# Performance work log

Hardware: AMD Instinct MI355X
Metric: run time of the kernel (lower is better)

The kernel has to match this reference:

```python
import jax, jax.numpy as jnp
import numpy as np
from jax import lax

SR = 16000
N_FFT = 400
HOP = 200
N_MELS = 128
HID = 128


def _mel_fb():
    # torchaudio melscale_fbanks defaults: htk scale, norm=None, f_min=0, f_max=sr/2
    all_freqs = np.linspace(0.0, SR / 2, N_FFT // 2 + 1)  # (201,)
    hz2mel = lambda f: 2595.0 * np.log10(1.0 + f / 700.0)
    mel2hz = lambda m: 700.0 * (10.0 ** (m / 2595.0) - 1.0)
    m_pts = np.linspace(hz2mel(0.0), hz2mel(SR / 2), N_MELS + 2)
    f_pts = mel2hz(m_pts)  # (130,)
    f_diff = np.diff(f_pts)  # (129,)
    slopes = f_pts[None, :] - all_freqs[:, None]  # (201,130)
    down = -slopes[:, :-2] / f_diff[:-1]
    up = slopes[:, 2:] / f_diff[1:]
    fb = np.maximum(0.0, np.minimum(down, up))  # (201,128)
    return jnp.asarray(fb, dtype=jnp.float32)

MEL_FB = _mel_fb()
HANN = jnp.asarray(np.hanning(N_FFT + 1)[:-1], dtype=jnp.float32)  # periodic hann(400)


def mel_spectrogram(x):
    # x: (B, T) waveform -> (B, n_mels, frames), power=2 mel spectrogram
    pad = N_FFT // 2
    xp = jnp.pad(x, ((0, 0), (pad, pad)), mode='reflect')
    n_frames = 1 + (xp.shape[1] - N_FFT) // HOP  # 81 for T=16000
    idx = jnp.arange(n_frames)[:, None] * HOP + jnp.arange(N_FFT)[None, :]
    frames = xp[:, idx] * HANN  # (B, frames, 400)
    spec = jnp.fft.rfft(frames, axis=-1)  # (B, frames, 201)
    power = jnp.abs(spec) ** 2
    mel = power @ MEL_FB  # (B, frames, 128)
    return jnp.transpose(mel, (0, 2, 1))  # (B, 128, frames)


def lstm_layer(x, W, U, b):
    # x: (B, T, F); gate order i, f, g, o (matches torch slicing)
    B = x.shape[0]
    h0 = jnp.zeros((B, HID), x.dtype)
    c0 = jnp.zeros((B, HID), x.dtype)

    def step(carry, x_t):
        h, c = carry
        gates = x_t @ W + h @ U + b  # (B, 4H)
        i = jax.nn.sigmoid(gates[:, :HID])
        f = jax.nn.sigmoid(gates[:, HID:2 * HID])
        g = jnp.tanh(gates[:, 2 * HID:3 * HID])
        o = jax.nn.sigmoid(gates[:, 3 * HID:])
        c = f * c + i * g
        h = o * jnp.tanh(c)
        return (h, c), h

    _, hs = lax.scan(step, (h0, c0), jnp.transpose(x, (1, 0, 2)))  # (T, B, H)
    return jnp.transpose(hs, (1, 0, 2))  # (B, T, H)


def setup_inputs() -> dict:
    key = jax.random.key(0)
    ks = jax.random.split(key, 16)
    s = 0.05
    return {
        'x': jax.random.normal(ks[0], (1024, 16000), dtype=jnp.float32),
        'conv_w': jax.random.normal(ks[1], (128, 128, 3), dtype=jnp.float32) * s,  # (out,in,k)
        'conv_b': jax.random.normal(ks[2], (128,), dtype=jnp.float32) * s,
        'W1': jax.random.normal(ks[3], (128, 4 * HID), dtype=jnp.float32) * s,
        'U1': jax.random.normal(ks[4], (HID, 4 * HID), dtype=jnp.float32) * s,
        'b1': jax.random.normal(ks[5], (4 * HID,), dtype=jnp.float32) * s,
        'W2': jax.random.normal(ks[6], (HID, 4 * HID), dtype=jnp.float32) * s,
        'U2': jax.random.normal(ks[7], (HID, 4 * HID), dtype=jnp.float32) * s,
        'b2': jax.random.normal(ks[8], (4 * HID,), dtype=jnp.float32) * s,
        'fc1_w': jax.random.normal(ks[9], (128, 128), dtype=jnp.float32) * s,  # (in,out)
        'fc1_b': jax.random.normal(ks[10], (128,), dtype=jnp.float32) * s,
        'proj_w': jax.random.normal(ks[11], (128, 35), dtype=jnp.float32) * s,  # (in,out)
        'proj_b': jax.random.normal(ks[12], (35,), dtype=jnp.float32) * s,
    }


def reference(x, conv_w, conv_b, W1, U1, b1, W2, U2, b2, fc1_w, fc1_b, proj_w, proj_b):
    # MelSpectrogram -> Conv1d(128,128,3) -> permute -> LSTM x2 -> fc1 -> mean(time) -> proj
    spec = mel_spectrogram(x)  # (B, 128, 81)
    conv = lax.conv_general_dilated(
        spec, conv_w, window_strides=(1,), padding='VALID',
        dimension_numbers=('NCH', 'OIH', 'NCH')) + conv_b[None, :, None]  # (B,128,79)
    h = jnp.transpose(conv, (0, 2, 1))  # (B, 79, 128)
    h = lstm_layer(h, W1, U1, b1)
    h = lstm_layer(h, W2, U2, b2)
    h = h @ fc1_w + fc1_b  # (B, 79, 128)
    h = jnp.mean(h, axis=1)  # (B, 128)
    return h @ proj_w + proj_b  # (B, 35)
```

## Files before the change

### kernel.cpp

```cpp
#include <hip/hip_runtime.h>
#include <math.h>

#define PI_D 3.14159265358979323846

#define BATCH   1024
#define TLEN    16000
#define NFFT    400
#define HOP     200
#define NFRAME  81
#define NBIN    201
#define NMEL    128
#define HID     128
#define TSTEPS  79
#define GATES   512

#define KDFT    416
#define NDFT    512
#define SINOFF  256
#define KPOW    224
#define KCONV   384
#define NCHUNK  2
#define CHROWS  (BATCH*NFRAME/NCHUNK)

static inline size_t al512(size_t v){ return (v + 511) & ~((size_t)511); }

__device__ __forceinline__ unsigned short bf_rne(float f){
    unsigned u = __float_as_uint(f);
    u += 0x7FFF + ((u >> 16) & 1);
    return (unsigned short)(u >> 16);
}
__device__ __forceinline__ void bf_split(float f, unsigned short& h, unsigned short& l){
    h = bf_rne(f);
    float hf = __uint_as_float(((unsigned)h) << 16);
    l = bf_rne(f - hf);
}
__device__ __forceinline__ void bf_split_fast(float f, unsigned short& h, unsigned short& l){
    unsigned u = __float_as_uint(f);
    h = (unsigned short)(u >> 16);
    float hf = __uint_as_float(u & 0xFFFF0000u);
    l = (unsigned short)(__float_as_uint(f - hf) >> 16);
}

__device__ __forceinline__ int kswz(int n, int k){
    return (k & ~31) | (((((k >> 3) & 3) ^ ((n >> 1) & 3))) << 3) | (k & 7);
}

typedef short bf16x8 __attribute__((ext_vector_type(8)));
typedef float f32x4  __attribute__((ext_vector_type(4)));
typedef unsigned short us8 __attribute__((ext_vector_type(8)));
typedef unsigned short us4 __attribute__((ext_vector_type(4)));
typedef _Float16 f16x8 __attribute__((ext_vector_type(8)));

__device__ __forceinline__ void gld16(const unsigned short* g, unsigned short* l){
    __builtin_amdgcn_global_load_lds(
        (const __attribute__((address_space(1))) unsigned int*)g,
        (__attribute__((address_space(3))) unsigned int*)l, 16, 0, 0);
}

__device__ __forceinline__ void barrier_lds(){
    __builtin_amdgcn_sched_barrier(0);
    asm volatile("s_waitcnt lgkmcnt(0)" ::: "memory");
    __builtin_amdgcn_s_barrier();
    __builtin_amdgcn_sched_barrier(0);
}

__global__ void setup_dft_t(unsigned short* __restrict__ th, unsigned short* __restrict__ tl){
    int idx = blockIdx.x*256 + threadIdx.x;
    if (idx >= NDFT*KDFT) return;
    int n = idx / KDFT, k = idx % KDFT;
    double v = 0.0;
    if (k < 400) {
        double w = 0.5 - 0.5*cos(2.0*PI_D*(double)k/400.0);
        if (n < NBIN)                              v = w * cos(2.0*PI_D*(double)((k*n)%400)/400.0);
        else if (n >= SINOFF && n < SINOFF + NBIN) v = w * sin(2.0*PI_D*(double)((k*(n-SINOFF))%400)/400.0);
    }
    unsigned short h, l; bf_split((float)v, h, l);
    int o = n*KDFT + kswz(n, k);
    th[o] = h; tl[o] = l;
}

__global__ void setup_fb_t(unsigned short* __restrict__ fh, unsigned short* __restrict__ fl){
    int idx = blockIdx.x*256 + threadIdx.x;
    if (idx >= NMEL*KPOW) return;
    int m = idx / KPOW, f = idx % KPOW;
    float v = 0.f;
    if (f < NBIN) {
        double melmax = 2595.0 * log10(1.0 + 8000.0/700.0);
        double p0 = 700.0*(pow(10.0, melmax*(double)(m  )/129.0/2595.0) - 1.0);
        double p1 = 700.0*(pow(10.0, melmax*(double)(m+1)/129.0/2595.0) - 1.0);
        double p2 = 700.0*(pow(10.0, melmax*(double)(m+2)/129.0/2595.0) - 1.0);
        double freq = 40.0 * (double)f;
        double dn = (freq - p0)/(p1 - p0);
        double up = (p2 - freq)/(p2 - p1);
        double t  = dn < up ? dn : up;
        if (t < 0.0) t = 0.0;
        v = (float)t;
    }
    unsigned short h, l; bf_split(v, h, l);
    int o = m*KPOW + kswz(m, f);
    fh[o] = h; fl[o] = l;
}

__global__ void setup_wc_t(unsigned short* __restrict__ wh, unsigned short* __restrict__ wl,
                           const float* __restrict__ cw){
    int idx = blockIdx.x*256 + threadIdx.x;
    if (idx >= NMEL*KCONV) return;
    int o = idx / KCONV, kk = idx % KCONV;
    int ksh = kk >> 7, i = kk & 127;
    unsigned short h, l; bf_split(cw[o*384 + i*3 + ksh], h, l);
    int p = o*KCONV + kswz(o, kk);
    wh[p] = h; wl[p] = l;
}

__global__ void setup_w_t(unsigned short* __restrict__ wh, unsigned short* __restrict__ wl,
                          const float* __restrict__ w){
    int idx = blockIdx.x*256 + threadIdx.x;
    if (idx >= GATES*HID) return;
    int c = idx / HID, i = idx % HID;
    unsigned short h, l; bf_split(w[(size_t)i*GATES + c], h, l);
    int p = c*HID + kswz(c, i);
    wh[p] = h; wl[p] = l;
}

__global__ void setup_comb(float* __restrict__ cwm, float* __restrict__ cb,
                           const float* __restrict__ fc1w, const float* __restrict__ fc1b,
                           const float* __restrict__ projw, const float* __restrict__ projb){
    int idx = blockIdx.x*256 + threadIdx.x;
    if (idx < 128*64) {
        int i = idx / 64, o = idx % 64;
        float v = 0.f;
        if (o < 35) {
            double s = 0.0;
            for (int m = 0; m < 128; m++) s += (double)fc1w[i*128+m] * (double)projw[m*35+o];
            v = (float)s;
        }
        cwm[idx] = v;
    } else if (idx < 128*64 + 64) {
        int o = idx - 128*64;
        float v = 0.f;
        if (o < 35) {
            double s = (double)projb[o];
            for (int m = 0; m < 128; m++) s += (double)fc1b[m] * (double)projw[m*35+o];
            v = (float)s;
        }
        cb[o] = v;
    }
}

__global__ void setup_uf(_Float16* __restrict__ uf, const float* __restrict__ u){
    int idx = blockIdx.x*256 + threadIdx.x;
    if (idx >= 65536) return;
    int j    = idx & 7;
    int lane = (idx >> 3) & 63;
    int nt   = (idx >> 9) & 7;
    int ks   = (idx >> 12) & 3;
    int w    = (idx >> 14) & 3;
    int k = ks*32 + (lane >> 4)*8 + j;
    int c = w*128 + nt*16 + (lane & 15);
    uf[idx] = (_Float16)u[(size_t)k*GATES + c];
}

enum AMode { A_NORMAL=0, A_FRAMES=1, A_POWER=2, A_CONV3=3 };

template<int AMODE, bool BIAS, int NT, bool WIDE>
__global__ __launch_bounds__(256)
void mgemm_k(const float* __restrict__ A,
             const unsigned short* __restrict__ BTh, const unsigned short* __restrict__ BTl,
             const float* __restrict__ bias, float* __restrict__ C,
             int Ksteps, int lda, int kstride, int ldc,
             const float* __restrict__ aux, int rowbase)
{
    constexpr int BM = WIDE ? 64 : 128;
    constexpr int BN = WIDE ? 256 : 128;
    constexpr int AP = BM / 32;
    __shared__ unsigned short Ash[2][BM][32], Asl[2][BM][32];
    __shared__ unsigned short Bsh[2][BN][32], Bsl[2][BN][32];

    const int nwg = gridDim.x;
    const int qq = nwg >> 3, rmd = nwg & 7;
    const int xcd = blockIdx.x & 7, loc = blockIdx.x >> 3;
    const int swz = (xcd < rmd ? xcd*(qq+1) : rmd*(qq+1) + (xcd - rmd)*qq) + loc;
    constexpr int LGNT = (NT == 4) ? 2 : (NT == 2) ? 1 : 0;
    const int m0 = (swz >> LGNT) * BM;
    const int n0 = (swz & (NT-1)) * BN;

    const int tid = threadIdx.x;
    const int lane = tid & 63, w = tid >> 6;
    const int wr = WIDE ? 0 : (w >> 1) * 64;
    const int wc = WIDE ? w * 64 : (w & 1) * 64;
    const int l15 = lane & 15;
    const int swf = ((lane & 15) >> 1) & 3;
    const int pos = (((lane >> 4) ^ swf) << 3);

    const int sr  = tid >> 3;
    const int wcol = (((((tid & 7) >> 1)) ^ ((tid >> 4) & 3)) << 3) + ((tid & 1) << 2);

    float va0[AP*4], vb0[AP*4], va1[AP*4], vb1[AP*4];

    auto issue_loads = [&](float (&va)[AP*4], float (&vb)[AP*4], int ksn){
        const int k0n = ksn * 32;
        #pragma unroll
        for (int p = 0; p < AP; p++) {
            const int row = p*32 + sr;
            const int kk = k0n + (tid & 7)*4;
            if constexpr (AMODE == A_NORMAL) {
                *(float4*)&va[p*4] = *(const float4*)(A + (size_t)(m0+row)*lda + kk);
            } else if constexpr (AMODE == A_POWER) {
                const float* src = A + (size_t)(m0+row)*lda + kk;
                *(float4*)&va[p*4] = *(const float4*)(src);
                *(float4*)&vb[p*4] = *(const float4*)(src + SINOFF);
            } else if constexpr (AMODE == A_FRAMES) {
                const int rr = rowbase + m0 + row;
                const int b = rr / NFRAME, f = rr - b*NFRAME;
                const float* xb = aux + (size_t)b * TLEN;
                const int q0 = f*HOP + kk - 200;
                if (q0 >= 0 && q0 + 3 < TLEN) {
                    *(float4*)&va[p*4] = *(const float4*)(xb + q0);
                } else {
                    #pragma unroll
                    for (int j = 0; j < 4; j++) {
                        int q = q0 + j;
                        if (q < 0) q = -q;
                        else if (q >= TLEN) q = 2*TLEN - 2 - q;
                        va[p*4+j] = xb[q];
                    }
                }
            } else {
                const int rr = m0 + row;
                const int b = rr / TSTEPS, t = rr - b*TSTEPS;
                const int ksh = kk >> 7, i = kk & 127;
                *(float4*)&va[p*4] = *(const float4*)(aux + ((size_t)(b*NFRAME + t + ksh)*NMEL + i));
            }
        }
        (void)vb;
    };
    auto write_stage = [&](float (&va)[AP*4], float (&vb)[AP*4], int wb){
        #pragma unroll
        for (int p = 0; p < AP; p++) {
            const int row = p*32 + sr;
            us4 hv, lv;
            #pragma unroll
            for (int j = 0; j < 4; j++) {
                float f = va[p*4+j];
                if constexpr (AMODE == A_POWER) f = f*f + vb[p*4+j]*vb[p*4+j];
                unsigned short h, l; bf_split_fast(f, h, l);
                hv[j] = h; lv[j] = l;
            }
            *(us4*)&Ash[wb][row][wcol] = hv;
            *(us4*)&Asl[wb][row][wcol] = lv;
        }
        (void)vb;
    };
    auto dma_b = [&](int wb, int ksn){
        const int k0n = ksn * 32;
        if constexpr (WIDE) {
            #pragma unroll
            for (int p = 0; p < 4; p++) {
                const int row = w*64 + p*16;
                const size_t o = (size_t)(n0 + row + (lane >> 2))*kstride + k0n + (lane & 3)*8;
                gld16(BTh + o, &Bsh[wb][row][0]);
                gld16(BTl + o, &Bsl[wb][row][0]);
            }
        } else {
            #pragma unroll
            for (int p = 0; p < 2; p++) {
                const int row = p*64 + w*16;
                const size_t o = (size_t)(n0 + row + (lane >> 2))*kstride + k0n + (lane & 3)*8;
                gld16(BTh + o, &Bsh[wb][row][0]);
                gld16(BTl + o, &Bsl[wb][row][0]);
            }
        }
    };

    f32x4 acc[4][4] = {};

    issue_loads(va1, vb1, 0);
    dma_b(0, 0);
    write_stage(va1, vb1, 0);
    issue_loads(va0, vb0, 1);
    __syncthreads();

    auto iter = [&](int ks, float (&vac)[AP*4], float (&vbc)[AP*4],
                    float (&vao)[AP*4], float (&vbo)[AP*4], int bufc){
        const bool pf1 = (ks + 1 < Ksteps);
        const bool pf2 = (ks + 2 < Ksteps);
        if (pf2) issue_loads(vao, vbo, ks + 2);
        if (pf1) dma_b(bufc ^ 1, ks + 1);

        bf16x8 ah[4], al[4];
        #pragma unroll
        for (int mt = 0; mt < 4; mt++) {
            ah[mt] = *(const bf16x8*)&Ash[bufc][wr + mt*16 + l15][pos];
            al[mt] = *(const bf16x8*)&Asl[bufc][wr + mt*16 + l15][pos];
        }
        #pragma unroll
        for (int nt = 0; nt < 4; nt++) {
            const int nr = wc + nt*16 + l15;
            bf16x8 bh = *(const bf16x8*)&Bsh[bufc][nr][pos];
            bf16x8 bl = *(const bf16x8*)&Bsl[bufc][nr][pos];
            #pragma unroll
            for (int mt = 0; mt < 4; mt++) {
                acc[mt][nt] = __builtin_amdgcn_mfma_f32_16x16x32_bf16(ah[mt], bh, acc[mt][nt], 0, 0, 0);
                acc[mt][nt] = __builtin_amdgcn_mfma_f32_16x16x32_bf16(ah[mt], bl, acc[mt][nt], 0, 0, 0);
                acc[mt][nt] = __builtin_amdgcn_mfma_f32_16x16x32_bf16(al[mt], bh, acc[mt][nt], 0, 0, 0);
            }
        }

        if (pf1) {
            write_stage(vac, vbc, bufc ^ 1);
            __syncthreads();
        }
    };

    for (int ks = 0; ks < Ksteps; ks += 2) {
        iter(ks, va0, vb0, va1, vb1, 0);
        if (ks + 1 < Ksteps) iter(ks + 1, va1, vb1, va0, vb0, 1);
    }

    const int quad = lane >> 4;
    #pragma unroll
    for (int nt = 0; nt < 4; nt++) {
        const int col = n0 + wc + (nt << 4) + l15;
        float b = 0.f;
        if constexpr (BIAS) b = bias[col];
        #pragma unroll
        for (int mt = 0; mt < 4; mt++) {
            #pragma unroll
            for (int r = 0; r < 4; r++) {
                const int row = m0 + wr + (mt << 4) + quad*4 + r;
                C[(size_t)row*ldc + col] = acc[mt][nt][r] + b;
            }
        }
    }
}

__global__ __launch_bounds__(256)
void gemm_small(const float* __restrict__ A, const float* __restrict__ Bm,
                const float* __restrict__ bias, float* __restrict__ C,
                int M, int N, int K, int lda, int ldb, int ldc)
{
    __shared__ float As[16][64+4];
    __shared__ float Bs[16][64];
    const int tid = threadIdx.x;
    const int tx = tid & 15, ty = tid >> 4;
    const int m0 = blockIdx.x * 64;
    float acc[4][4] = {{0,0,0,0},{0,0,0,0},{0,0,0,0},{0,0,0,0}};
    const int am = tid >> 2, ak = (tid & 3) * 4;
    const int bk = tid >> 4, bn = (tid & 15) * 4;
    for (int k0 = 0; k0 < K; k0 += 16) {
        float4 av = *(const float4*)(A + (size_t)(m0+am)*lda + k0 + ak);
        As[ak+0][am]=av.x; As[ak+1][am]=av.y; As[ak+2][am]=av.z; As[ak+3][am]=av.w;
        *(float4*)&Bs[bk][bn] = *(const float4*)(Bm + (size_t)(k0+bk)*ldb + bn);
        __syncthreads();
        #pragma unroll
        for (int k = 0; k < 16; k++) {
            float4 a = *(const float4*)&As[k][ty*4];
            float4 b = *(const float4*)&Bs[k][tx*4];
            #pragma unroll
            for (int i = 0; i < 4; i++) {
                float av_ = ((const float*)&a)[i];
                acc[i][0] = fmaf(av_, b.x, acc[i][0]);
                acc[i][1] = fmaf(av_, b.y, acc[i][1]);
                acc[i][2] = fmaf(av_, b.z, acc[i][2]);
                acc[i][3] = fmaf(av_, b.w, acc[i][3]);
            }
        }
        __syncthreads();
    }
    #pragma unroll
    for (int ir = 0; ir < 4; ir++) {
        const int row = m0 + ty*4 + ir;
        #pragma unroll
        for (int jc = 0; jc < 4; jc++) {
            const int col = tx*4 + jc;
            if (col < N) C[(size_t)row*ldc + col] = acc[ir][jc] + bias[col];
        }
    }
}

__device__ __forceinline__ float sigm_f(float x){ return 1.f/(1.f + __expf(-x)); }
__device__ __forceinline__ float tanh_f(float x){ float e = __expf(2.f*x); return 1.f - 2.f/(e + 1.f); }

#define LROWS 2
#define LTHREADS 256
#define HPAD 136

__global__ __launch_bounds__(LTHREADS, 2)
void lstm_k(const float* __restrict__ X, const _Float16* __restrict__ Uf, float* __restrict__ H)
{
    __shared__ _Float16 hsA[16*HPAD];
    __shared__ float gs[GATES*5];
    const int tid = threadIdx.x;
    const int b0 = blockIdx.x * LROWS;
    const int lane = tid & 63, w = tid >> 6;
    const int m16 = lane & 15, quad = lane >> 4;
    const int r = tid >> 7;
    const int j = tid & 127;

    f32x4 bfr[4][8];
    #pragma unroll
    for (int ks = 0; ks < 4; ks++)
        #pragma unroll
        for (int nt = 0; nt < 8; nt++) {
            bfr[ks][nt] = *(const f32x4*)(Uf + ((((w*4 + ks)*8 + nt)*64 + lane) << 3));
            asm volatile("" : "+v"(bfr[ks][nt]));
        }

    for (int i = tid; i < 16*HPAD; i += LTHREADS) hsA[i] = (_Float16)0.f;
    float cst = 0.f;
    const float* xb = X + ((size_t)(b0 + r)*TSTEPS)*GATES + j;
    __syncthreads();

    float xi = xb[0], xf = xb[128], xg = xb[256], xo = xb[384];

    for (int t = 0; t < TSTEPS; t++) {
        float xi_n = 0.f, xf_n = 0.f, xg_n = 0.f, xo_n = 0.f;
        if (t + 1 < TSTEPS) {
            const float* xp = xb + (size_t)(t + 1)*GATES;
            xi_n = xp[0]; xf_n = xp[128]; xg_n = xp[256]; xo_n = xp[384];
        }

        f16x8 ah[4];
        #pragma unroll
        for (int ks = 0; ks < 4; ks++)
            ah[ks] = *(const f16x8*)&hsA[m16*HPAD + ks*32 + quad*8];

        f32x4 acc[8] = {};
        #pragma unroll
        for (int ks = 0; ks < 4; ks++)
            #pragma unroll
            for (int nt = 0; nt < 8; nt++)
                acc[nt] = __builtin_amdgcn_mfma_f32_16x16x32_f16(
                    ah[ks], __builtin_bit_cast(f16x8, bfr[ks][nt]), acc[nt], 0, 0, 0);

        if (quad == 0) {
            #pragma unroll
            for (int nt = 0; nt < 8; nt++) {
                const int c = w*128 + nt*16 + m16;
                #pragma unroll
                for (int rr = 0; rr < LROWS; rr++) gs[c*5 + rr] = acc[nt][rr];
            }
        }
        barrier_lds();

        {
            const float gi = gs[(      j)*5 + r] + xi;
            const float gf = gs[(128 + j)*5 + r] + xf;
            const float gg = gs[(256 + j)*5 + r] + xg;
            const float go = gs[(384 + j)*5 + r] + xo;
            const float cn = sigm_f(gf)*cst + sigm_f(gi)*tanh_f(gg);
            cst = cn;
            const float hn = sigm_f(go)*tanh_f(cn);
            H[((size_t)(b0 + r)*TSTEPS + t)*HID + j] = hn;
            hsA[r*HPAD + j] = (_Float16)hn;
        }
        barrier_lds();

        xi = xi_n; xf = xf_n; xg = xg_n; xo = xo_n;
    }
}

__global__ void mean_k(const float* __restrict__ H, float* __restrict__ Mh){
    const int idx = blockIdx.x*256 + threadIdx.x;
    if (idx >= BATCH*HID) return;
    const int b = idx >> 7, j = idx & 127;
    const float* p = H + (size_t)b*TSTEPS*HID + j;
    float s = 0.f;
    for (int t = 0; t < TSTEPS; t++) s += p[(size_t)t*HID];
    Mh[idx] = s * (1.0f/(float)TSTEPS);
}

extern "C" void kernel_launch(void* const* d_in, const int* in_sizes, int n_in,
                              void* d_out, int out_size, void* d_ws, size_t ws_size,
                              hipStream_t stream)
{
    const float* x      = (const float*)d_in[0];
    const float* conv_w = (const float*)d_in[1];
    const float* conv_b = (const float*)d_in[2];
    const float* W1     = (const float*)d_in[3];
    const float* U1     = (const float*)d_in[4];
    const float* b1     = (const float*)d_in[5];
    const float* W2     = (const float*)d_in[6];
    const float* U2     = (const float*)d_in[7];
    const float* b2     = (const float*)d_in[8];
    const float* fc1_w  = (const float*)d_in[9];
    const float* fc1_b  = (const float*)d_in[10];
    const float* proj_w = (const float*)d_in[11];
    const float* proj_b = (const float*)d_in[12];
    float* out = (float*)d_out;

    char* ws = (char*)d_ws;
    size_t off = 0;
    unsigned short* Tth = (unsigned short*)(ws + off); off = al512(off + (size_t)NDFT*KDFT*2);
    unsigned short* Ttl = (unsigned short*)(ws + off); off = al512(off + (size_t)NDFT*KDFT*2);
    unsigned short* fbh = (unsigned short*)(ws + off); off = al512(off + (size_t)NMEL*KPOW*2);
    unsigned short* fbl = (unsigned short*)(ws + off); off = al512(off + (size_t)NMEL*KPOW*2);
    unsigned short* wch = (unsigned short*)(ws + off); off = al512(off + (size_t)NMEL*KCONV*2);
    unsigned short* wcl = (unsigned short*)(ws + off); off = al512(off + (size_t)NMEL*KCONV*2);
    unsigned short* w1h = (unsigned short*)(ws + off); off = al512(off + (size_t)GATES*HID*2);
    unsigned short* w1l = (unsigned short*)(ws + off); off = al512(off + (size_t)GATES*HID*2);
    unsigned short* w2h = (unsigned short*)(ws + off); off = al512(off + (size_t)GATES*HID*2);
    unsigned short* w2l = (unsigned short*)(ws + off); off = al512(off + (size_t)GATES*HID*2);
    float* Cw   = (float*)(ws + off); off = al512(off + (size_t)128*64*4);
    float* Cb   = (float*)(ws + off); off = al512(off + (size_t)64*4);
    float* Mh   = (float*)(ws + off); off = al512(off + (size_t)BATCH*HID*4);
    _Float16* Uf1 = (_Float16*)(ws + off); off = al512(off + (size_t)65536*2);
    _Float16* Uf2 = (_Float16*)(ws + off); off = al512(off + (size_t)65536*2);
    float* MEL  = (float*)(ws + off); off = al512(off + (size_t)BATCH*NFRAME*NMEL*4);
    float* CONV = (float*)(ws + off); off = al512(off + (size_t)BATCH*TSTEPS*NMEL*4);
    float* X    = (float*)(ws + off); off = al512(off + (size_t)BATCH*TSTEPS*GATES*4);
    float* DFT = X;
    float* H1  = MEL;
    float* H2  = CONV;
    (void)ws_size; (void)out_size; (void)n_in; (void)in_sizes;

    setup_dft_t<<<(NDFT*KDFT + 255)/256, 256, 0, stream>>>(Tth, Ttl);
    setup_fb_t <<<(NMEL*KPOW + 255)/256, 256, 0, stream>>>(fbh, fbl);
    setup_wc_t <<<(NMEL*KCONV + 255)/256, 256, 0, stream>>>(wch, wcl, conv_w);
    setup_w_t  <<<(GATES*HID + 255)/256, 256, 0, stream>>>(w1h, w1l, W1);
    setup_w_t  <<<(GATES*HID + 255)/256, 256, 0, stream>>>(w2h, w2l, W2);
    setup_comb <<<(128*64 + 64 + 255)/256, 256, 0, stream>>>(Cw, Cb, fc1_w, fc1_b, proj_w, proj_b);
    setup_uf   <<<65536/256, 256, 0, stream>>>(Uf1, U1);
    setup_uf   <<<65536/256, 256, 0, stream>>>(Uf2, U2);

    for (int ch = 0; ch < NCHUNK; ch++) {
        const int rowbase = ch * CHROWS;
        mgemm_k<A_FRAMES,false,2,true><<<(CHROWS/64)*2, 256, 0, stream>>>(
            nullptr, Tth, Ttl, nullptr, DFT, KDFT/32, 0, KDFT, NDFT, x, rowbase);
        mgemm_k<A_POWER,false,1,false><<<CHROWS/128, 256, 0, stream>>>(
            DFT, fbh, fbl, nullptr, MEL + (size_t)rowbase*NMEL, KPOW/32, NDFT, KPOW, NMEL, nullptr, 0);
    }

    mgemm_k<A_CONV3,true,1,false><<<BATCH*TSTEPS/128, 256, 0, stream>>>(
        nullptr, wch, wcl, conv_b, CONV, KCONV/32, 0, KCONV, NMEL, MEL, 0);

    mgemm_k<A_NORMAL,true,2,true><<<(BATCH*TSTEPS/64)*2, 256, 0, stream>>>(
        CONV, w1h, w1l, b1, X, HID/32, NMEL, HID, GATES, nullptr, 0);
    lstm_k<<<BATCH/LROWS, LTHREADS, 0, stream>>>(X, Uf1, H1);

    mgemm_k<A_NORMAL,true,2,true><<<(BATCH*TSTEPS/64)*2, 256, 0, stream>>>(
        H1, w2h, w2l, b2, X, HID/32, HID, HID, GATES, nullptr, 0);
    lstm_k<<<BATCH/LROWS, LTHREADS, 0, stream>>>(X, Uf2, H2);

    mean_k<<<(BATCH*HID + 255)/256, 256, 0, stream>>>(H2, Mh);
    gemm_small<<<BATCH/64, 256, 0, stream>>>(Mh, Cw, Cb, out, BATCH, 35, HID, HID, 64, 35);
}
```

Baseline: 665.4 us.

## Interleave LSTM gate columns and process 16 rows per block in registers

Permutes the gate columns of W, U and the biases so each thread's MFMA accumulators hold the i,f,g,o values for the same hidden unit. The cell update can then run straight from registers, with no gate staging through shared memory. The LSTM block now covers 16 batch rows instead of 2, using the full 16-row MFMA tile rather than a mostly empty one. It also double-buffers h in LDS so each step needs one barrier instead of two. In exchange the grid shrinks from 512 to 64 blocks, which leaves many CUs idle on a large GPU.

```diff
diff --git a/kernel.cpp b/kernel.cpp
--- a/kernel.cpp
+++ b/kernel.cpp
@@ -116,10 +116,20 @@
                           const float* __restrict__ w){
     int idx = blockIdx.x*256 + threadIdx.x;
     if (idx >= GATES*HID) return;
-    int c = idx / HID, i = idx % HID;
+    int cp = idx / HID, i = idx % HID;
+    int c = (cp & 3)*128 + (cp >> 2);
     unsigned short h, l; bf_split(w[(size_t)i*GATES + c], h, l);
-    int p = c*HID + kswz(c, i);
+    int p = cp*HID + kswz(cp, i);
     wh[p] = h; wl[p] = l;
+}
+
+__global__ void setup_pb(float* __restrict__ pb1, float* __restrict__ pb2,
+                         const float* __restrict__ b1, const float* __restrict__ b2){
+    int cp = blockIdx.x*256 + threadIdx.x;
+    if (cp >= GATES) return;
+    int c = (cp & 3)*128 + (cp >> 2);
+    pb1[cp] = b1[c];
+    pb2[cp] = b2[c];
 }
 
 __global__ void setup_comb(float* __restrict__ cwm, float* __restrict__ cb,
@@ -150,14 +160,16 @@
 __global__ void setup_uf(_Float16* __restrict__ uf, const float* __restrict__ u){
     int idx = blockIdx.x*256 + threadIdx.x;
     if (idx >= 65536) return;
-    int j    = idx & 7;
+    int jj   = idx & 7;
     int lane = (idx >> 3) & 63;
     int nt   = (idx >> 9) & 7;
     int ks   = (idx >> 12) & 3;
     int w    = (idx >> 14) & 3;
-    int k = ks*32 + (lane >> 4)*8 + j;
-    int c = w*128 + nt*16 + (lane & 15);
-    uf[idx] = (_Float16)u[(size_t)k*GATES + c];
+    int f = w*8 + nt;
+    int g = f & 3;
+    int jcol = (f >> 2)*16 + (lane & 15);
+    int k = ks*32 + (lane >> 4)*8 + jj;
+    uf[idx] = (_Float16)u[(size_t)k*GATES + g*128 + jcol];
 }
 
 enum AMode { A_NORMAL=0, A_FRAMES=1, A_POWER=2, A_CONV3=3 };
@@ -381,21 +393,19 @@
 __device__ __forceinline__ float sigm_f(float x){ return 1.f/(1.f + __expf(-x)); }
 __device__ __forceinline__ float tanh_f(float x){ float e = __expf(2.f*x); return 1.f - 2.f/(e + 1.f); }
 
-#define LROWS 2
+#define LROWS 16
 #define LTHREADS 256
 #define HPAD 136
 
-__global__ __launch_bounds__(LTHREADS, 2)
+__global__ __launch_bounds__(LTHREADS, 1)
 void lstm_k(const float* __restrict__ X, const _Float16* __restrict__ Uf, float* __restrict__ H)
 {
-    __shared__ _Float16 hsA[16*HPAD];
-    __shared__ float gs[GATES*5];
+    __shared__ _Float16 hsA[2][16*HPAD];
     const int tid = threadIdx.x;
     const int b0 = blockIdx.x * LROWS;
     const int lane = tid & 63, w = tid >> 6;
-    const int m16 = lane & 15, quad = lane >> 4;
-    const int r = tid >> 7;
-    const int j = tid & 127;
+    const int l15 = lane & 15, quad = lane >> 4;
+    const int jc0 = 32*w + l15;
 
     f32x4 bfr[4][8];
     #pragma unroll
@@ -406,24 +416,36 @@
             asm volatile("" : "+v"(bfr[ks][nt]));
         }
 
-    for (int i = tid; i < 16*HPAD; i += LTHREADS) hsA[i] = (_Float16)0.f;
-    float cst = 0.f;
-    const float* xb = X + ((size_t)(b0 + r)*TSTEPS)*GATES + j;
+    {
+        _Float16* hz = &hsA[0][0];
+        for (int i = tid; i < 2*16*HPAD; i += LTHREADS) hz[i] = (_Float16)0.f;
+    }
+
+    float cst[8] = {0,0,0,0,0,0,0,0};
+    const float* xp[4];
+    float* hp[4];
+    #pragma unroll
+    for (int rr = 0; rr < 4; rr++) {
+        const int br = b0 + quad*4 + rr;
+        xp[rr] = X + (size_t)br*TSTEPS*GATES + jc0*4;
+        hp[rr] = H + (size_t)br*TSTEPS*HID;
+    }
     __syncthreads();
 
-    float xi = xb[0], xf = xb[128], xg = xb[256], xo = xb[384];
+    float4 xv[8];
+    #pragma unroll
+    for (int rr = 0; rr < 4; rr++)
+        #pragma unroll
+        for (int jgl = 0; jgl < 2; jgl++)
+            xv[rr*2+jgl] = *(const float4*)(xp[rr] + jgl*64);
 
     for (int t = 0; t < TSTEPS; t++) {
-        float xi_n = 0.f, xf_n = 0.f, xg_n = 0.f, xo_n = 0.f;
-        if (t + 1 < TSTEPS) {
-            const float* xp = xb + (size_t)(t + 1)*GATES;
-            xi_n = xp[0]; xf_n = xp[128]; xg_n = xp[256]; xo_n = xp[384];
-        }
+        const int p = t & 1;
 
         f16x8 ah[4];
         #pragma unroll
         for (int ks = 0; ks < 4; ks++)
-            ah[ks] = *(const f16x8*)&hsA[m16*HPAD + ks*32 + quad*8];
+            ah[ks] = *(const f16x8*)&hsA[p][l15*HPAD + ks*32 + quad*8];
 
         f32x4 acc[8] = {};
         #pragma unroll
@@ -433,30 +455,32 @@
                 acc[nt] = __builtin_amdgcn_mfma_f32_16x16x32_f16(
                     ah[ks], __builtin_bit_cast(f16x8, bfr[ks][nt]), acc[nt], 0, 0, 0);
 
-        if (quad == 0) {
-            #pragma unroll
-            for (int nt = 0; nt < 8; nt++) {
-                const int c = w*128 + nt*16 + m16;
+        #pragma unroll
+        for (int jgl = 0; jgl < 2; jgl++) {
+            #pragma unroll
+            for (int rr = 0; rr < 4; rr++) {
+                const float4 xg = xv[rr*2+jgl];
+                const float gi = acc[jgl*4+0][rr] + xg.x;
+                const float gf = acc[jgl*4+1][rr] + xg.y;
+                const float gg = acc[jgl*4+2][rr] + xg.z;
+                const float go = acc[jgl*4+3][rr] + xg.w;
+                const float cn = sigm_f(gf)*cst[rr*2+jgl] + sigm_f(gi)*tanh_f(gg);
+                cst[rr*2+jgl] = cn;
+                const float hn = sigm_f(go)*tanh_f(cn);
+                hp[rr][(size_t)t*HID + jc0 + jgl*16] = hn;
+                hsA[p^1][(quad*4+rr)*HPAD + jc0 + jgl*16] = (_Float16)hn;
+            }
+        }
+
+        if (t + 1 < TSTEPS) {
+            #pragma unroll
+            for (int rr = 0; rr < 4; rr++)
                 #pragma unroll
-                for (int rr = 0; rr < LROWS; rr++) gs[c*5 + rr] = acc[nt][rr];
-            }
-        }
+                for (int jgl = 0; jgl < 2; jgl++)
+                    xv[rr*2+jgl] = *(const float4*)(xp[rr] + (size_t)(t+1)*GATES + jgl*64);
+        }
+
         barrier_lds();
-
-        {
-            const float gi = gs[(      j)*5 + r] + xi;
-            const float gf = gs[(128 + j)*5 + r] + xf;
-            const float gg = gs[(256 + j)*5 + r] + xg;
-            const float go = gs[(384 + j)*5 + r] + xo;
-            const float cn = sigm_f(gf)*cst + sigm_f(gi)*tanh_f(gg);
-            cst = cn;
-            const float hn = sigm_f(go)*tanh_f(cn);
-            H[((size_t)(b0 + r)*TSTEPS + t)*HID + j] = hn;
-            hsA[r*HPAD + j] = (_Float16)hn;
-        }
-        barrier_lds();
-
-        xi = xi_n; xf = xf_n; xg = xg_n; xo = xo_n;
     }
 }
 
@@ -503,6 +527,8 @@
     unsigned short* w2l = (unsigned short*)(ws + off); off = al512(off + (size_t)GATES*HID*2);
     float* Cw   = (float*)(ws + off); off = al512(off + (size_t)128*64*4);
     float* Cb   = (float*)(ws + off); off = al512(off + (size_t)64*4);
+    float* Pb1  = (float*)(ws + off); off = al512(off + (size_t)GATES*4);
+    float* Pb2  = (float*)(ws + off); off = al512(off + (size_t)GATES*4);
     float* Mh   = (float*)(ws + off); off = al512(off + (size_t)BATCH*HID*4);
     _Float16* Uf1 = (_Float16*)(ws + off); off = al512(off + (size_t)65536*2);
     _Float16* Uf2 = (_Float16*)(ws + off); off = al512(off + (size_t)65536*2);
@@ -519,6 +545,7 @@
     setup_wc_t <<<(NMEL*KCONV + 255)/256, 256, 0, stream>>>(wch, wcl, conv_w);
     setup_w_t  <<<(GATES*HID + 255)/256, 256, 0, stream>>>(w1h, w1l, W1);
     setup_w_t  <<<(GATES*HID + 255)/256, 256, 0, stream>>>(w2h, w2l, W2);
+    setup_pb   <<<(GATES + 255)/256, 256, 0, stream>>>(Pb1, Pb2, b1, b2);
     setup_comb <<<(128*64 + 64 + 255)/256, 256, 0, stream>>>(Cw, Cb, fc1_w, fc1_b, proj_w, proj_b);
     setup_uf   <<<65536/256, 256, 0, stream>>>(Uf1, U1);
     setup_uf   <<<65536/256, 256, 0, stream>>>(Uf2, U2);
@@ -535,11 +562,11 @@
         nullptr, wch, wcl, conv_b, CONV, KCONV/32, 0, KCONV, NMEL, MEL, 0);
 
     mgemm_k<A_NORMAL,true,2,true><<<(BATCH*TSTEPS/64)*2, 256, 0, stream>>>(
-        CONV, w1h, w1l, b1, X, HID/32, NMEL, HID, GATES, nullptr, 0);
+        CONV, w1h, w1l, Pb1, X, HID/32, NMEL, HID, GATES, nullptr, 0);
     lstm_k<<<BATCH/LROWS, LTHREADS, 0, stream>>>(X, Uf1, H1);
 
     mgemm_k<A_NORMAL,true,2,true><<<(BATCH*TSTEPS/64)*2, 256, 0, stream>>>(
-        H1, w2h, w2l, b2, X, HID/32, HID, HID, GATES, nullptr, 0);
+        H1, w2h, w2l, Pb2, X, HID/32, HID, HID, GATES, nullptr, 0);
     lstm_k<<<BATCH/LROWS, LTHREADS, 0, stream>>>(X, Uf2, H2);
 
     mean_k<<<(BATCH*HID + 255)/256, 256, 0, stream>>>(H2, Mh);
```

Result: slower. 832.7 us (+25.1%).

## Interleave cos/sin DFT columns and fuse power computation into DFT GEMM epilogue

Applied to the files above, without the earlier changes.

The DFT basis now interleaves cosine and sine columns per bin, so each adjacent lane pair holds the real and imaginary parts. The DFT GEMM epilogue combines them with a lane shuffle and writes |X|^2 directly into a compact 224-wide power buffer. The mel GEMM then reads that buffer as a plain matrix instead of loading two 512-wide halves and squaring on the fly. This cuts the intermediate write and read traffic to about half. The two-chunk split is dropped in favour of single full-size launches.

```diff
diff --git a/kernel.cpp b/kernel.cpp
--- a/kernel.cpp
+++ b/kernel.cpp
@@ -13,14 +13,13 @@
 #define HID     128
 #define TSTEPS  79
 #define GATES   512
+#define TOTROWS (BATCH*NFRAME)
 
 #define KDFT    416
 #define NDFT    512
-#define SINOFF  256
 #define KPOW    224
+#define LPOW    224
 #define KCONV   384
-#define NCHUNK  2
-#define CHROWS  (BATCH*NFRAME/NCHUNK)
 
 static inline size_t al512(size_t v){ return (v + 511) & ~((size_t)511); }
 
@@ -69,10 +68,11 @@
     if (idx >= NDFT*KDFT) return;
     int n = idx / KDFT, k = idx % KDFT;
     double v = 0.0;
-    if (k < 400) {
+    if (k < 400 && n < 402) {
         double w = 0.5 - 0.5*cos(2.0*PI_D*(double)k/400.0);
-        if (n < NBIN)                              v = w * cos(2.0*PI_D*(double)((k*n)%400)/400.0);
-        else if (n >= SINOFF && n < SINOFF + NBIN) v = w * sin(2.0*PI_D*(double)((k*(n-SINOFF))%400)/400.0);
+        int bin = n >> 1;
+        if ((n & 1) == 0) v = w * cos(2.0*PI_D*(double)((k*bin)%400)/400.0);
+        else              v = w * sin(2.0*PI_D*(double)((k*bin)%400)/400.0);
     }
     unsigned short h, l; bf_split((float)v, h, l);
     int o = n*KDFT + kswz(n, k);
@@ -160,9 +160,9 @@
     uf[idx] = (_Float16)u[(size_t)k*GATES + c];
 }
 
-enum AMode { A_NORMAL=0, A_FRAMES=1, A_POWER=2, A_CONV3=3 };
-
-template<int AMODE, bool BIAS, int NT, bool WIDE>
+enum AMode { A_NORMAL=0, A_FRAMES=1, A_CONV3=3 };
+
+template<int AMODE, bool BIAS, int NT, bool WIDE, bool PEPI>
 __global__ __launch_bounds__(256)
 void mgemm_k(const float* __restrict__ A,
              const unsigned short* __restrict__ BTh, const unsigned short* __restrict__ BTl,
@@ -195,9 +195,9 @@
     const int sr  = tid >> 3;
     const int wcol = (((((tid & 7) >> 1)) ^ ((tid >> 4) & 3)) << 3) + ((tid & 1) << 2);
 
-    float va0[AP*4], vb0[AP*4], va1[AP*4], vb1[AP*4];
-
-    auto issue_loads = [&](float (&va)[AP*4], float (&vb)[AP*4], int ksn){
+    float va0[AP*4], va1[AP*4];
+
+    auto issue_loads = [&](float (&va)[AP*4], int ksn){
         const int k0n = ksn * 32;
         #pragma unroll
         for (int p = 0; p < AP; p++) {
@@ -205,10 +205,6 @@
             const int kk = k0n + (tid & 7)*4;
             if constexpr (AMODE == A_NORMAL) {
                 *(float4*)&va[p*4] = *(const float4*)(A + (size_t)(m0+row)*lda + kk);
-            } else if constexpr (AMODE == A_POWER) {
-                const float* src = A + (size_t)(m0+row)*lda + kk;
-                *(float4*)&va[p*4] = *(const float4*)(src);
-                *(float4*)&vb[p*4] = *(const float4*)(src + SINOFF);
             } else if constexpr (AMODE == A_FRAMES) {
                 const int rr = rowbase + m0 + row;
                 const int b = rr / NFRAME, f = rr - b*NFRAME;
@@ -232,24 +228,20 @@
                 *(float4*)&va[p*4] = *(const float4*)(aux + ((size_t)(b*NFRAME + t + ksh)*NMEL + i));
             }
         }
-        (void)vb;
     };
-    auto write_stage = [&](float (&va)[AP*4], float (&vb)[AP*4], int wb){
+    auto write_stage = [&](float (&va)[AP*4], int wb){
         #pragma unroll
         for (int p = 0; p < AP; p++) {
             const int row = p*32 + sr;
             us4 hv, lv;
             #pragma unroll
             for (int j = 0; j < 4; j++) {
-                float f = va[p*4+j];
-                if constexpr (AMODE == A_POWER) f = f*f + vb[p*4+j]*vb[p*4+j];
-                unsigned short h, l; bf_split_fast(f, h, l);
+                unsigned short h, l; bf_split_fast(va[p*4+j], h, l);
                 hv[j] = h; lv[j] = l;
             }
             *(us4*)&Ash[wb][row][wcol] = hv;
             *(us4*)&Asl[wb][row][wcol] = lv;
         }
-        (void)vb;
     };
     auto dma_b = [&](int wb, int ksn){
         const int k0n = ksn * 32;
@@ -274,17 +266,16 @@
 
     f32x4 acc[4][4] = {};
 
-    issue_loads(va1, vb1, 0);
+    issue_loads(va1, 0);
     dma_b(0, 0);
-    write_stage(va1, vb1, 0);
-    issue_loads(va0, vb0, 1);
+    write_stage(va1, 0);
+    issue_loads(va0, 1);
     __syncthreads();
 
-    auto iter = [&](int ks, float (&vac)[AP*4], float (&vbc)[AP*4],
-                    float (&vao)[AP*4], float (&vbo)[AP*4], int bufc){
+    auto iter = [&](int ks, float (&vac)[AP*4], float (&vao)[AP*4], int bufc){
         const bool pf1 = (ks + 1 < Ksteps);
         const bool pf2 = (ks + 2 < Ksteps);
-        if (pf2) issue_loads(vao, vbo, ks + 2);
+        if (pf2) issue_loads(vao, ks + 2);
         if (pf1) dma_b(bufc ^ 1, ks + 1);
 
         bf16x8 ah[4], al[4];
@@ -307,28 +298,50 @@
         }
 
         if (pf1) {
-            write_stage(vac, vbc, bufc ^ 1);
+            write_stage(vac, bufc ^ 1);
             __syncthreads();
         }
     };
 
     for (int ks = 0; ks < Ksteps; ks += 2) {
-        iter(ks, va0, vb0, va1, vb1, 0);
-        if (ks + 1 < Ksteps) iter(ks + 1, va1, vb1, va0, vb0, 1);
+        iter(ks, va0, va1, 0);
+        if (ks + 1 < Ksteps) iter(ks + 1, va1, va0, 1);
     }
 
     const int quad = lane >> 4;
-    #pragma unroll
-    for (int nt = 0; nt < 4; nt++) {
-        const int col = n0 + wc + (nt << 4) + l15;
-        float b = 0.f;
-        if constexpr (BIAS) b = bias[col];
-        #pragma unroll
-        for (int mt = 0; mt < 4; mt++) {
-            #pragma unroll
-            for (int r = 0; r < 4; r++) {
-                const int row = m0 + wr + (mt << 4) + quad*4 + r;
-                C[(size_t)row*ldc + col] = acc[mt][nt][r] + b;
+    if constexpr (PEPI) {
+        #pragma unroll
+        for (int nt = 0; nt < 4; nt++) {
+            const int col = n0 + wc + (nt << 4) + l15;
+            #pragma unroll
+            for (int mt = 0; mt < 4; mt++) {
+                #pragma unroll
+                for (int r = 0; r < 4; r++) {
+                    const int row = m0 + wr + (mt << 4) + quad*4 + r;
+                    const float v = acc[mt][nt][r];
+                    const float u = __shfl_xor(v, 1);
+                    if (!(l15 & 1)) {
+                        if (col < 402)
+                            C[(size_t)row*ldc + (col >> 1)] = v*v + u*u;
+                        else if (col < 448)
+                            C[(size_t)row*ldc + (col >> 1)] = 0.f;
+                    }
+                }
+            }
+        }
+    } else {
+        #pragma unroll
+        for (int nt = 0; nt < 4; nt++) {
+            const int col = n0 + wc + (nt << 4) + l15;
+            float b = 0.f;
+            if constexpr (BIAS) b = bias[col];
+            #pragma unroll
+            for (int mt = 0; mt < 4; mt++) {
+                #pragma unroll
+                for (int r = 0; r < 4; r++) {
+                    const int row = m0 + wr + (mt << 4) + quad*4 + r;
+                    C[(size_t)row*ldc + col] = acc[mt][nt][r] + b;
+                }
             }
         }
     }
@@ -509,7 +522,7 @@
     float* MEL  = (float*)(ws + off); off = al512(off + (size_t)BATCH*NFRAME*NMEL*4);
     float* CONV = (float*)(ws + off); off = al512(off + (size_t)BATCH*TSTEPS*NMEL*4);
     float* X    = (float*)(ws + off); off = al512(off + (size_t)BATCH*TSTEPS*GATES*4);
-    float* DFT = X;
+    float* POW = X;
     float* H1  = MEL;
     float* H2  = CONV;
     (void)ws_size; (void)out_size; (void)n_in; (void)in_sizes;
@@ -523,22 +536,19 @@
     setup_uf   <<<65536/256, 256, 0, stream>>>(Uf1, U1);
     setup_uf   <<<65536/256, 256, 0, stream>>>(Uf2, U2);
 
-    for (int ch = 0; ch < NCHUNK; ch++) {
-        const int rowbase = ch * CHROWS;
-        mgemm_k<A_FRAMES,false,2,true><<<(CHROWS/64)*2, 256, 0, stream>>>(
-            nullptr, Tth, Ttl, nullptr, DFT, KDFT/32, 0, KDFT, NDFT, x, rowbase);
-        mgemm_k<A_POWER,false,1,false><<<CHROWS/128, 256, 0, stream>>>(
-            DFT, fbh, fbl, nullptr, MEL + (size_t)rowbase*NMEL, KPOW/32, NDFT, KPOW, NMEL, nullptr, 0);
-    }
-
-    mgemm_k<A_CONV3,true,1,false><<<BATCH*TSTEPS/128, 256, 0, stream>>>(
+    mgemm_k<A_FRAMES,false,2,true,true><<<(TOTROWS/64)*2, 256, 0, stream>>>(
+        nullptr, Tth, Ttl, nullptr, POW, KDFT/32, 0, KDFT, LPOW, x, 0);
+    mgemm_k<A_NORMAL,false,1,false,false><<<TOTROWS/128, 256, 0, stream>>>(
+        POW, fbh, fbl, nullptr, MEL, KPOW/32, LPOW, KPOW, NMEL, nullptr, 0);
+
+    mgemm_k<A_CONV3,true,1,false,false><<<BATCH*TSTEPS/128, 256, 0, stream>>>(
         nullptr, wch, wcl, conv_b, CONV, KCONV/32, 0, KCONV, NMEL, MEL, 0);
 
-    mgemm_k<A_NORMAL,true,2,true><<<(BATCH*TSTEPS/64)*2, 256, 0, stream>>>(
+    mgemm_k<A_NORMAL,true,2,true,false><<<(BATCH*TSTEPS/64)*2, 256, 0, stream>>>(
         CONV, w1h, w1l, b1, X, HID/32, NMEL, HID, GATES, nullptr, 0);
     lstm_k<<<BATCH/LROWS, LTHREADS, 0, stream>>>(X, Uf1, H1);
 
-    mgemm_k<A_NORMAL,true,2,true><<<(BATCH*TSTEPS/64)*2, 256, 0, stream>>>(
+    mgemm_k<A_NORMAL,true,2,true,false><<<(BATCH*TSTEPS/64)*2, 256, 0, stream>>>(
         H1, w2h, w2l, b2, X, HID/32, HID, HID, GATES, nullptr, 0);
     lstm_k<<<BATCH/LROWS, LTHREADS, 0, stream>>>(X, Uf2, H2);
 
```

Result: faster. 648.0 us, median of 2 (-2.6%).
